# Optimization experiments

Measured on AMD Instinct MI355X. Metric: run time of the kernel, lower is better.

Reference implementation:

```python
import jax, jax.numpy as jnp
import numpy as np

ACTION_NS = [3, 3, 2, 4, 24]        # forward_back, left_right, jump, sneak_sprint, attack_...
RANGE_STARTS = [6, 8, 10, 11, 14]   # action_ranges starts (indices 0..5 are commit + camera ops)
N_ACTIONS = 37
LOGIT_DIM = 36
MIN_DELTA = 0.5 / 2**3
MAX_STEP = 20
MAX_CAMSTEP = 6
B, NUM_INPUT, HIDDEN = 32768, 1024, 2048
D_IN = NUM_INPUT + 4 + LOGIT_DIM


def setup_inputs():
    key = jax.random.key(0)
    ks = jax.random.split(key, 12)
    inp = {
        "fc_input": jax.random.normal(ks[0], (B, NUM_INPUT), jnp.float32),
        "camera": jax.random.normal(ks[1], (B, 2), jnp.float32),
        "rand_u": jax.random.uniform(ks[2], (B,), jnp.float32),
        "W1": (jax.random.normal(ks[3], (D_IN, HIDDEN), jnp.float32) / np.sqrt(D_IN)).astype(jnp.float32),
        "b1": jnp.zeros((HIDDEN,), jnp.float32),
        "W2": (jax.random.normal(ks[4], (HIDDEN, N_ACTIONS), jnp.float32) / np.sqrt(HIDDEN)).astype(jnp.float32),
        "b2": jnp.zeros((N_ACTIONS,), jnp.float32),
    }
    names = ["act_fb", "act_lr", "act_jp", "act_ss", "act_atk"]
    for i, (nm, n) in enumerate(zip(names, ACTION_NS)):
        inp[nm] = jax.random.randint(ks[5 + i], (B,), 0, n, jnp.int32)
    return inp


def _discretize_scan(camera, acts):
    # Faithful jax version of the 20-step no_grad target/input construction loop.
    nB = camera.shape[0]
    cam0, cam1 = camera[:, 0], camera[:, 1]

    def step(carry, _):
        ac, delta, rdac, dch, cam_steps, committed, norm = carry
        oh = [jax.nn.one_hot(r, n, dtype=jnp.float32) for r, n in zip(rdac, ACTION_NS)]
        inp_vec = jnp.concatenate([ac] + oh + [delta[:, None], dch.astype(jnp.float32)[:, None]], axis=1)  # [B,40]
        norm = norm + (~committed).astype(jnp.float32)
        commit = ((jnp.abs(cam0) < 1e-5) & (jnp.abs(cam1) < 1e-5)) | (cam_steps >= MAX_CAMSTEP)
        for r, a in zip(rdac, acts):
            commit = commit & (r == a)
        dac = jnp.zeros((nB,), jnp.int32)
        modified = commit
        new_rdac = []
        for r, a, rs in zip(rdac, acts, RANGE_STARTS):
            disc = (~modified) & (r != a)
            dac = jnp.where(disc & (a == 0), r - 1 + rs, jnp.where(disc, a - 1 + rs, dac))
            new_rdac.append(jnp.where(disc, a, r))
            modified = modified | disc
        d2 = delta * 2.0
        # NOTE: original torch code compares cam[:,1] against ac[:,0]; bug preserved.
        dmask = (~modified) & (~dch) & ((jnp.abs(cam0 - ac[:, 0]) > d2) | (jnp.abs(cam1 - ac[:, 0]) > d2))
        dac = jnp.where(dmask, 5, dac)
        delta = jnp.where(dmask, jnp.clip(d2, -0.5, 0.5), delta)
        modified = modified | dmask
        sx = jnp.where(cam0 < ac[:, 0], -1.0, 1.0)
        sy = jnp.where(cam1 < ac[:, 1], -1.0, 1.0)
        quad = jnp.where(sx < 0, jnp.where(sy < 0, 1, 3), jnp.where(sy < 0, 2, 4)).astype(jnp.int32)
        dac = jnp.where(~modified, quad, dac)
        move = jnp.stack([sx, sy], axis=1) * delta[:, None]
        ac = jnp.where((~modified)[:, None], ac + move, ac)
        delta = jnp.where(~modified, delta * 0.5, delta)
        dch = dch | (~modified)
        cam_steps = cam_steps + (~modified).astype(jnp.int32)
        committed = committed | commit
        return (ac, delta, tuple(new_rdac), dch, cam_steps, committed, norm), (inp_vec, dac)

    init = (jnp.zeros((nB, 2), jnp.float32),
            jnp.full((nB,), MIN_DELTA, jnp.float32),
            tuple(jnp.zeros((nB,), jnp.int32) for _ in ACTION_NS),
            jnp.zeros((nB,), bool),
            jnp.zeros((nB,), jnp.int32),
            jnp.zeros((nB,), bool),
            jnp.zeros((nB,), jnp.float32))
    carry, (all_inputs, all_dacs) = jax.lax.scan(step, init, None, length=MAX_STEP)
    return all_inputs, all_dacs, carry[-1]  # [T,B,40], [T,B], norm [B]


def reference(fc_input, camera, rand_u, W1, b1, W2, b2, act_fb, act_lr, act_jp, act_ss, act_atk):
    acts = (act_fb, act_lr, act_jp, act_ss, act_atk)
    all_inputs, all_dacs, norm = _discretize_scan(camera, acts)
    rand_sam = jnp.minimum((rand_u * norm).astype(jnp.int32), MAX_STEP - 1)  # sample an uncommitted step
    idx = jnp.arange(fc_input.shape[0])
    sel = jax.lax.stop_gradient(all_inputs[rand_sam, idx])  # [B,40]
    tgt = jax.lax.stop_gradient(all_dacs[rand_sam, idx])    # [B]
    x = jnp.concatenate([fc_input, sel], axis=1)
    h = x @ W1 + b1
    h = h * jax.nn.sigmoid(h)  # swish
    logits = h @ W2 + b2
    logp = jax.nn.log_softmax(logits, axis=-1)
    loss = -jnp.take_along_axis(logp, tgt[:, None], axis=1)[:, 0]  # per-sample CE (reduction='none')
    return loss
```

## Files before the change

### kernel.cpp

```cpp
#include <hip/hip_runtime.h>
#include <hip/hip_bf16.h>
#include <stdint.h>

#define B_ROWS 32768
#define NUM_IN 1024
#define D_PAD2 1088
#define HID    2048
#define NPAD   64

typedef __attribute__((ext_vector_type(8))) short bf16x8;
typedef __attribute__((ext_vector_type(4))) float f32x4;
typedef unsigned short ushort_t;

__device__ __forceinline__ unsigned short f2bf(float f){
  union { float f; uint32_t u; } x; x.f = f;
  uint32_t u = x.u;
  return (unsigned short)((u + 0x7FFFu + ((u >> 16) & 1u)) >> 16);
}

__device__ __forceinline__ void gload16(const void* g, void* l){
  __builtin_amdgcn_global_load_lds((const __attribute__((address_space(1))) void*)g,
                                   (__attribute__((address_space(3))) void*)l, 16, 0, 0);
}

__device__ __forceinline__ int disc_step(
    float cam0, float cam1, const int a[5],
    float& ac0, float& ac1, float& delta,
    int r[5], bool& dch, int& cam_steps, bool& committed, float& norm)
{
  const int RS[5] = {6, 8, 10, 11, 14};
  norm += committed ? 0.0f : 1.0f;
  bool commit = ((fabsf(cam0) < 1e-5f) && (fabsf(cam1) < 1e-5f)) || (cam_steps >= 6);
  #pragma unroll
  for (int i = 0; i < 5; ++i) commit = commit && (r[i] == a[i]);
  int dac = 0;
  bool modified = commit;
  #pragma unroll
  for (int i = 0; i < 5; ++i){
    bool disc = (!modified) && (r[i] != a[i]);
    if (disc){
      dac = (a[i] == 0) ? (r[i] - 1 + RS[i]) : (a[i] - 1 + RS[i]);
      r[i] = a[i];
      modified = true;
    }
  }
  float d2 = delta * 2.0f;
  bool dmask = (!modified) && (!dch) &&
               ((fabsf(cam0 - ac0) > d2) || (fabsf(cam1 - ac0) > d2));
  if (dmask){ dac = 5; delta = fminf(d2, 0.5f); modified = true; }
  if (!modified){
    float sx = (cam0 < ac0) ? -1.0f : 1.0f;
    float sy = (cam1 < ac1) ? -1.0f : 1.0f;
    dac = (sx < 0.0f) ? ((sy < 0.0f) ? 1 : 3) : ((sy < 0.0f) ? 2 : 4);
    ac0 += sx * delta; ac1 += sy * delta;
    delta *= 0.5f;
    dch = true;
    cam_steps += 1;
  }
  committed = committed || commit;
  return dac;
}

__global__ void k_prep(const float* __restrict__ fc, const float* __restrict__ W1,
                       const float* __restrict__ W2,
                       const float* __restrict__ camera, const float* __restrict__ rand_u,
                       const int* __restrict__ afb, const int* __restrict__ alr,
                       const int* __restrict__ ajp, const int* __restrict__ ass,
                       const int* __restrict__ aat,
                       unsigned short* __restrict__ xb, unsigned short* __restrict__ w1t,
                       unsigned short* __restrict__ w2t, int* __restrict__ tgt)
{
  __shared__ float lt[64][65];
  const int b = blockIdx.x;
  const int tid = threadIdx.x;
  if (b < 16384){
    int gid = b * 256 + tid;
    int row = gid >> 7;
    int c   = gid & 127;
    const float4* p = (const float4*)(fc + (size_t)row * NUM_IN + c * 8);
    float4 f0 = p[0], f1 = p[1];
    uint4 pk;
    pk.x = (uint32_t)f2bf(f0.x) | ((uint32_t)f2bf(f0.y) << 16);
    pk.y = (uint32_t)f2bf(f0.z) | ((uint32_t)f2bf(f0.w) << 16);
    pk.z = (uint32_t)f2bf(f1.x) | ((uint32_t)f2bf(f1.y) << 16);
    pk.w = (uint32_t)f2bf(f1.z) | ((uint32_t)f2bf(f1.w) << 16);
    *(uint4*)(xb + (size_t)row * D_PAD2 + c * 8) = pk;
    return;
  }
  if (b < 16928){
    const int bi = b - 16384;
    const int kt = bi % 17, nt = bi / 17;
    const int k0 = kt * 64, n0 = nt * 64;
    const int c = tid & 63, rq = tid >> 6;
    #pragma unroll
    for (int rr = 0; rr < 16; ++rr){
      const int r = rr * 4 + rq;
      const int k = k0 + r;
      lt[r][c] = (k < 1064) ? W1[(size_t)k * HID + n0 + c] : 0.0f;
    }
    __syncthreads();
    #pragma unroll
    for (int rr = 0; rr < 16; ++rr){
      const int r = rr * 4 + rq;
      w1t[(size_t)(n0 + r) * D_PAD2 + k0 + c] = f2bf(lt[c][r]);
    }
    return;
  }
  if (b < 17440){
    int idx = (b - 16928) * 256 + tid;
    int n = idx >> 11;
    int k = idx & (HID - 1);
    float v = (n < 37) ? W2[(size_t)k * 37 + n] : 0.0f;
    w2t[idx] = f2bf(v);
    return;
  }
  int row = (b - 17440) * 256 + tid;
  float cam0 = camera[2*row], cam1 = camera[2*row + 1];
  int a[5] = { afb[row], alr[row], ajp[row], ass[row], aat[row] };

  float ac0 = 0.f, ac1 = 0.f, delta = 0.0625f, norm = 0.f;
  int r[5] = {0,0,0,0,0};
  bool dch = false, committed = false; int cam_steps = 0;
  for (int t = 0; t < 20; ++t)
    disc_step(cam0, cam1, a, ac0, ac1, delta, r, dch, cam_steps, committed, norm);

  int rs = (int)(rand_u[row] * norm);
  if (rs > 19) rs = 19;
  if (rs < 0) rs = 0;

  ac0 = 0.f; ac1 = 0.f; delta = 0.0625f; norm = 0.f;
  r[0]=r[1]=r[2]=r[3]=r[4]=0; dch = false; committed = false; cam_steps = 0;
  for (int t = 0; t < rs; ++t)
    disc_step(cam0, cam1, a, ac0, ac1, delta, r, dch, cam_steps, committed, norm);

  float vec[40];
  #pragma unroll
  for (int j = 0; j < 40; ++j) vec[j] = 0.0f;
  vec[0] = ac0; vec[1] = ac1;
  const int offs[5] = {2, 5, 8, 10, 14};
  #pragma unroll
  for (int i = 0; i < 5; ++i) vec[offs[i] + r[i]] = 1.0f;
  vec[38] = delta; vec[39] = dch ? 1.0f : 0.0f;

  int dac = disc_step(cam0, cam1, a, ac0, ac1, delta, r, dch, cam_steps, committed, norm);
  tgt[row] = dac;

  unsigned short* o = xb + (size_t)row * D_PAD2 + NUM_IN;
  #pragma unroll
  for (int j = 0; j < 40; ++j) o[j] = f2bf(vec[j]);
  #pragma unroll
  for (int j = 40; j < 64; ++j) o[j] = 0;
}

#define LDS_A0 0
#define LDS_A1 16384
#define LDS_B0 32768
#define LDS_B1 49152

#define STAGE(G, REG, ROW0, KT, HALF) do { \
    const ushort_t* s0_ = (G) + (size_t)((ROW0) + (HALF)*128 + srow) * D_PAD2 + ((KT) << 6) + scol; \
    gload16(s0_, lds + (REG) + (HALF)*8192 + t*8); \
    gload16(s0_ + (size_t)64 * D_PAD2, lds + (REG) + (HALF)*8192 + 4096 + t*8); \
  } while(0)

#define LDA_(REG, MH) do { \
    _Pragma("unroll") for (int mi_ = 0; mi_ < 4; ++mi_){ \
      const int row_ = arow_base + (MH)*64 + mi_*16; \
      _Pragma("unroll") for (int kk_ = 0; kk_ < 2; ++kk_) \
        aR[mi_][kk_] = *(const bf16x8*)(lds + (REG) + row_*64 + (((kk_*4+lg)^axor)<<3)); \
    } \
  } while(0)

#define LDB_(REG, NH, BR) do { \
    _Pragma("unroll") for (int ni_ = 0; ni_ < 2; ++ni_){ \
      const int row_ = brow_base + (NH)*32 + ni_*16; \
      _Pragma("unroll") for (int kk_ = 0; kk_ < 2; ++kk_) \
        BR[ni_][kk_] = *(const bf16x8*)(lds + (REG) + row_*64 + (((kk_*4+lg)^axor)<<3)); \
    } \
  } while(0)

#define MMA(MH, NH, BR) do { \
    __builtin_amdgcn_s_setprio(1); \
    _Pragma("unroll") for (int mi_ = 0; mi_ < 4; ++mi_) \
    _Pragma("unroll") for (int ni_ = 0; ni_ < 2; ++ni_) \
    _Pragma("unroll") for (int kk_ = 0; kk_ < 2; ++kk_) \
      acc[(MH)*4+mi_][(NH)*2+ni_] = __builtin_amdgcn_mfma_f32_16x16x32_bf16( \
          aR[mi_][kk_], BR[ni_][kk_], acc[(MH)*4+mi_][(NH)*2+ni_], 0, 0, 0); \
    __builtin_amdgcn_s_setprio(0); \
  } while(0)

#define BAR() __builtin_amdgcn_s_barrier()
#define LGKM0()      asm volatile("s_waitcnt lgkmcnt(0)" ::: "memory")
#define WAIT_VM6()   asm volatile("s_waitcnt vmcnt(6)" ::: "memory")
#define WAIT_VM0()   asm volatile("s_waitcnt vmcnt(0)" ::: "memory")

__global__ __launch_bounds__(512, 2) void k_gemm1(const ushort_t* __restrict__ xb,
                                                  const ushort_t* __restrict__ w1t,
                                                  const ushort_t* __restrict__ w2t,
                                                  const float* __restrict__ b1,
                                                  float* __restrict__ pbuf)
{
  __shared__ ushort_t lds[65536];
  const int t = threadIdx.x;
  const int lane = t & 63;
  const int wid = t >> 6, wm = wid >> 2, wn = wid & 3;
  const int lr = lane & 15, lg = lane >> 4;

  const int bid = blockIdx.x;
  const int swz = (bid & 7) * 128 + (bid >> 3);
  const int brow = (swz >> 3) << 8;
  const int bcol = (swz & 7) << 8;

  const int srow = t >> 3;
  const int scol = ((t & 7) ^ (srow & 7)) << 3;

  const int axor = lr & 7;
  const int arow_base = wm*128 + lr;
  const int brow_base = wn*64 + lr;

  f32x4 acc[8][4] = {};
  bf16x8 aR[4][2], bR0[2][2], bR1[2][2];

  STAGE(xb,  LDS_A0, brow, 0, 0);  STAGE(xb,  LDS_A0, brow, 0, 1);
  STAGE(w1t, LDS_B0, bcol, 0, 0);  STAGE(w1t, LDS_B0, bcol, 0, 1);
  STAGE(xb,  LDS_A1, brow, 1, 0);
  STAGE(w1t, LDS_B1, bcol, 1, 0);  STAGE(w1t, LDS_B1, bcol, 1, 1);
  WAIT_VM6();
  BAR();

  for (int i = 0; i < 8; ++i){
    const int c1 = 2*i + 1;
    const int n0 = 2*i + 2;
    const int n1 = (2*i + 3 <= 16) ? 2*i + 3 : 16;

    LDA_(LDS_A0, 0); LDB_(LDS_B0, 0, bR0); LDB_(LDS_B0, 1, bR1);
    STAGE(xb, LDS_A1, brow, c1, 1);
    BAR(); LGKM0();
    MMA(0, 0, bR0);
    BAR();
    STAGE(w1t, LDS_B0, bcol, n0, 0);
    BAR();
    MMA(0, 1, bR1);
    BAR();
    LDA_(LDS_A0, 1);
    STAGE(w1t, LDS_B0, bcol, n0, 1);
    BAR(); LGKM0();
    MMA(1, 0, bR0);
    BAR();
    STAGE(xb, LDS_A0, brow, n0, 0);
    WAIT_VM6();
    BAR();
    MMA(1, 1, bR1);
    BAR();
    LDA_(LDS_A1, 0); LDB_(LDS_B1, 0, bR0); LDB_(LDS_B1, 1, bR1);
    STAGE(xb, LDS_A0, brow, n0, 1);
    BAR(); LGKM0();
    MMA(0, 0, bR0);
    BAR();
    STAGE(w1t, LDS_B1, bcol, n1, 0);
    BAR();
    MMA(0, 1, bR1);
    BAR();
    LDA_(LDS_A1, 1);
    STAGE(w1t, LDS_B1, bcol, n1, 1);
    BAR(); LGKM0();
    MMA(1, 0, bR0);
    BAR();
    STAGE(xb, LDS_A1, brow, n1, 0);
    WAIT_VM6();
    BAR();
    MMA(1, 1, bR1);
    BAR();
  }

  LDA_(LDS_A0, 0); LDB_(LDS_B0, 0, bR0); LDB_(LDS_B0, 1, bR1);
  LGKM0();
  MMA(0, 0, bR0); MMA(0, 1, bR1);
  LDA_(LDS_A0, 1);
  LGKM0();
  MMA(1, 0, bR0); MMA(1, 1, bR1);

  bf16x8 w2fA[4][4];
  #pragma unroll
  for (int ks = 0; ks < 4; ++ks)
    #pragma unroll
    for (int ni = 0; ni < 4; ++ni)
      w2fA[ks][ni] = *(const bf16x8*)(w2t + (size_t)(ni*16 + lr) * HID + bcol + ks*32 + lg*8);

  WAIT_VM0();
  BAR();

  float b1v[4];
  #pragma unroll
  for (int ni = 0; ni < 4; ++ni) b1v[ni] = b1[bcol + wn*64 + ni*16 + lr];

  #pragma unroll
  for (int mi = 0; mi < 8; ++mi){
    #pragma unroll
    for (int ni = 0; ni < 4; ++ni){
      const int col = wn*64 + ni*16 + lr;
      #pragma unroll
      for (int i2 = 0; i2 < 4; ++i2){
        const int row = wm*128 + mi*16 + lg*4 + i2;
        float v = acc[mi][ni][i2] + b1v[ni];
        float s = v / (1.0f + __expf(-v));
        const int chunk = (col >> 3) ^ (row & 7);
        lds[row*256 + chunk*8 + (col & 7)] = f2bf(s);
      }
    }
  }
  __syncthreads();

  bf16x8 w2fB[4][4];
  #pragma unroll
  for (int ks = 0; ks < 4; ++ks)
    #pragma unroll
    for (int ni = 0; ni < 4; ++ni)
      w2fB[ks][ni] = *(const bf16x8*)(w2t + (size_t)(ni*16 + lr) * HID + bcol + (ks+4)*32 + lg*8);

  const int rb = wid * 32;
  f32x4 acc2[2][4] = {};
  #pragma unroll
  for (int ks = 0; ks < 8; ++ks){
    bf16x8 a2[2];
    #pragma unroll
    for (int m = 0; m < 2; ++m){
      const int row = rb + m*16 + lr;
      a2[m] = *(const bf16x8*)(lds + row*256 + (((ks*4+lg) ^ (lr & 7)) << 3));
    }
    #pragma unroll
    for (int m = 0; m < 2; ++m)
      #pragma unroll
      for (int ni = 0; ni < 4; ++ni)
        acc2[m][ni] = __builtin_amdgcn_mfma_f32_16x16x32_bf16(
            a2[m], (ks < 4) ? w2fA[ks & 3][ni] : w2fB[ks & 3][ni], acc2[m][ni], 0, 0, 0);
  }

  const int cb = bcol >> 8;
  #pragma unroll
  for (int m = 0; m < 2; ++m)
    #pragma unroll
    for (int ni = 0; ni < 4; ++ni)
      #pragma unroll
      for (int i2 = 0; i2 < 4; ++i2){
        const int r = brow + rb + m*16 + lg*4 + i2;
        pbuf[((size_t)cb << 21) + ((size_t)r << 6) + ni*16 + lr] = acc2[m][ni][i2];
      }
}

__global__ __launch_bounds__(256) void k_red(const float* __restrict__ pbuf,
                                             const float* __restrict__ b2,
                                             const int* __restrict__ tgt,
                                             float* __restrict__ loss)
{
  const int lane = threadIdx.x & 63, w = threadIdx.x >> 6;
  const int row0 = blockIdx.x * 128 + w * 32;
  const float bias = (lane < 37) ? b2[lane] : 0.0f;
  for (int i = 0; i < 32; ++i){
    const int r = row0 + i;
    float s = 0.0f;
    #pragma unroll
    for (int cb = 0; cb < 8; ++cb)
      s += pbuf[((size_t)cb << 21) + ((size_t)r << 6) + lane];
    float x = (lane < 37) ? (s + bias) : -1e30f;
    float m = x;
    #pragma unroll
    for (int off = 1; off < 64; off <<= 1) m = fmaxf(m, __shfl_xor(m, off, 64));
    float e = __expf(x - m);
    float se = e;
    #pragma unroll
    for (int off = 1; off < 64; off <<= 1) se += __shfl_xor(se, off, 64);
    const int tg = tgt[r];
    const float pick = __shfl(x, tg, 64);
    if (lane == 0) loss[r] = m + __logf(se) - pick;
  }
}

extern "C" void kernel_launch(void* const* d_in, const int* in_sizes, int n_in,
                              void* d_out, int out_size, void* d_ws, size_t ws_size,
                              hipStream_t stream)
{
  (void)in_sizes; (void)n_in; (void)out_size; (void)ws_size;
  const float* fc  = (const float*)d_in[0];
  const float* cam = (const float*)d_in[1];
  const float* ru  = (const float*)d_in[2];
  const float* W1  = (const float*)d_in[3];
  const float* b1  = (const float*)d_in[4];
  const float* W2  = (const float*)d_in[5];
  const float* b2  = (const float*)d_in[6];
  const int* afb = (const int*)d_in[7];
  const int* alr = (const int*)d_in[8];
  const int* ajp = (const int*)d_in[9];
  const int* ass = (const int*)d_in[10];
  const int* aat = (const int*)d_in[11];
  float* loss = (float*)d_out;

  char* ws = (char*)d_ws;
  unsigned short* xb  = (unsigned short*)(ws);
  unsigned short* w1t = (unsigned short*)(ws + 71303168);
  unsigned short* w2t = (unsigned short*)(ws + 75759616);
  int*            tgt = (int*)           (ws + 76021760);
  float*          pbuf= (float*)         (ws + 76152832);

  k_prep<<<17568, 256, 0, stream>>>(fc, W1, W2, cam, ru, afb, alr, ajp, ass, aat,
                                    xb, w1t, w2t, tgt);
  k_gemm1<<<(B_ROWS/256) * (HID/256), 512, 0, stream>>>(xb, w1t, w2t, b1, pbuf);
  k_red  <<<B_ROWS / 128, 256, 0, stream>>>(pbuf, b2, tgt, loss);
}
```

Baseline: 269.6 us.

## Reschedule GEMM1 LDS loads and global staging; precompute swizzled LDS base pointers

The k-loop schedule of the first GEMM is reworked. Per-lane swizzled LDS base addresses are computed once as byte pointers, so each fragment load becomes a base plus a constant offset. Loads of the second B fragment half are deferred to the phase that consumes them, and A-tile staging moves into the loop so each sub-phase issues one global-to-LDS copy. Wait counts change to vmcnt(4), with an lgkmcnt(8) partial wait added. The goal is to spread memory traffic more evenly between MFMA bursts and cut address arithmetic, at the risk of exposing load latency or creating subtle LDS reuse hazards.

```diff
diff --git a/kernel.cpp b/kernel.cpp
--- a/kernel.cpp
+++ b/kernel.cpp
@@ -163,20 +163,16 @@
     gload16(s0_ + (size_t)64 * D_PAD2, lds + (REG) + (HALF)*8192 + 4096 + t*8); \
   } while(0)
 
-#define LDA_(REG, MH) do { \
-    _Pragma("unroll") for (int mi_ = 0; mi_ < 4; ++mi_){ \
-      const int row_ = arow_base + (MH)*64 + mi_*16; \
-      _Pragma("unroll") for (int kk_ = 0; kk_ < 2; ++kk_) \
-        aR[mi_][kk_] = *(const bf16x8*)(lds + (REG) + row_*64 + (((kk_*4+lg)^axor)<<3)); \
-    } \
+#define LDA_(BUF, MH) do { \
+    _Pragma("unroll") for (int mi_ = 0; mi_ < 4; ++mi_) \
+    _Pragma("unroll") for (int kk_ = 0; kk_ < 2; ++kk_) \
+      aR[mi_][kk_] = *(const bf16x8*)(aBk[kk_] + (BUF)*32768 + ((MH)*64 + mi_*16)*128); \
   } while(0)
 
-#define LDB_(REG, NH, BR) do { \
-    _Pragma("unroll") for (int ni_ = 0; ni_ < 2; ++ni_){ \
-      const int row_ = brow_base + (NH)*32 + ni_*16; \
-      _Pragma("unroll") for (int kk_ = 0; kk_ < 2; ++kk_) \
-        BR[ni_][kk_] = *(const bf16x8*)(lds + (REG) + row_*64 + (((kk_*4+lg)^axor)<<3)); \
-    } \
+#define LDB_(BUF, NH, BR) do { \
+    _Pragma("unroll") for (int ni_ = 0; ni_ < 2; ++ni_) \
+    _Pragma("unroll") for (int kk_ = 0; kk_ < 2; ++kk_) \
+      BR[ni_][kk_] = *(const bf16x8*)(bBk[kk_] + (BUF)*32768 + ((NH)*32 + ni_*16)*128); \
   } while(0)
 
 #define MMA(MH, NH, BR) do { \
@@ -190,9 +186,10 @@
   } while(0)
 
 #define BAR() __builtin_amdgcn_s_barrier()
-#define LGKM0()      asm volatile("s_waitcnt lgkmcnt(0)" ::: "memory")
-#define WAIT_VM6()   asm volatile("s_waitcnt vmcnt(6)" ::: "memory")
-#define WAIT_VM0()   asm volatile("s_waitcnt vmcnt(0)" ::: "memory")
+#define LGKM0()    asm volatile("s_waitcnt lgkmcnt(0)" ::: "memory")
+#define LGKM8()    asm volatile("s_waitcnt lgkmcnt(8)" ::: "memory")
+#define WAIT_VM4() asm volatile("s_waitcnt vmcnt(4)" ::: "memory")
+#define WAIT_VM0() asm volatile("s_waitcnt vmcnt(0)" ::: "memory")
 
 __global__ __launch_bounds__(512, 2) void k_gemm1(const ushort_t* __restrict__ xb,
                                                   const ushort_t* __restrict__ w1t,
@@ -218,14 +215,20 @@
   const int arow_base = wm*128 + lr;
   const int brow_base = wn*64 + lr;
 
+  const char* aBk[2];
+  const char* bBk[2];
+  aBk[0] = (const char*)lds + arow_base*128 + (((0*4+lg)^axor) << 4);
+  aBk[1] = (const char*)lds + arow_base*128 + (((1*4+lg)^axor) << 4);
+  bBk[0] = (const char*)lds + 65536 + brow_base*128 + (((0*4+lg)^axor) << 4);
+  bBk[1] = (const char*)lds + 65536 + brow_base*128 + (((1*4+lg)^axor) << 4);
+
   f32x4 acc[8][4] = {};
   bf16x8 aR[4][2], bR0[2][2], bR1[2][2];
 
   STAGE(xb,  LDS_A0, brow, 0, 0);  STAGE(xb,  LDS_A0, brow, 0, 1);
   STAGE(w1t, LDS_B0, bcol, 0, 0);  STAGE(w1t, LDS_B0, bcol, 0, 1);
-  STAGE(xb,  LDS_A1, brow, 1, 0);
   STAGE(w1t, LDS_B1, bcol, 1, 0);  STAGE(w1t, LDS_B1, bcol, 1, 1);
-  WAIT_VM6();
+  WAIT_VM4();
   BAR();
 
   for (int i = 0; i < 8; ++i){
@@ -233,50 +236,54 @@
     const int n0 = 2*i + 2;
     const int n1 = (2*i + 3 <= 16) ? 2*i + 3 : 16;
 
-    LDA_(LDS_A0, 0); LDB_(LDS_B0, 0, bR0); LDB_(LDS_B0, 1, bR1);
+    LDA_(0, 0); LDB_(0, 0, bR0);
+    STAGE(xb, LDS_A1, brow, c1, 0);
+    LGKM8();
+    BAR(); LGKM0();
+    MMA(0, 0, bR0);
+    BAR();
+    LDB_(0, 1, bR1);
     STAGE(xb, LDS_A1, brow, c1, 1);
     BAR(); LGKM0();
+    MMA(0, 1, bR1);
+    BAR();
+    LDA_(0, 1);
+    STAGE(w1t, LDS_B0, bcol, n0, 0);
+    BAR(); LGKM0();
+    MMA(1, 0, bR0);
+    BAR();
+    STAGE(w1t, LDS_B0, bcol, n0, 1);
+    WAIT_VM4();
+    BAR();
+    MMA(1, 1, bR1);
+    BAR();
+    LDA_(1, 0); LDB_(1, 0, bR0);
+    STAGE(xb, LDS_A0, brow, n0, 0);
+    LGKM8();
+    BAR(); LGKM0();
     MMA(0, 0, bR0);
     BAR();
-    STAGE(w1t, LDS_B0, bcol, n0, 0);
-    BAR();
+    LDB_(1, 1, bR1);
+    STAGE(xb, LDS_A0, brow, n0, 1);
+    BAR(); LGKM0();
     MMA(0, 1, bR1);
     BAR();
-    LDA_(LDS_A0, 1);
-    STAGE(w1t, LDS_B0, bcol, n0, 1);
+    LDA_(1, 1);
+    STAGE(w1t, LDS_B1, bcol, n1, 0);
     BAR(); LGKM0();
     MMA(1, 0, bR0);
     BAR();
-    STAGE(xb, LDS_A0, brow, n0, 0);
-    WAIT_VM6();
+    STAGE(w1t, LDS_B1, bcol, n1, 1);
+    WAIT_VM4();
     BAR();
     MMA(1, 1, bR1);
     BAR();
-    LDA_(LDS_A1, 0); LDB_(LDS_B1, 0, bR0); LDB_(LDS_B1, 1, bR1);
-    STAGE(xb, LDS_A0, brow, n0, 1);
-    BAR(); LGKM0();
-    MMA(0, 0, bR0);
-    BAR();
-    STAGE(w1t, LDS_B1, bcol, n1, 0);
-    BAR();
-    MMA(0, 1, bR1);
-    BAR();
-    LDA_(LDS_A1, 1);
-    STAGE(w1t, LDS_B1, bcol, n1, 1);
-    BAR(); LGKM0();
-    MMA(1, 0, bR0);
-    BAR();
-    STAGE(xb, LDS_A1, brow, n1, 0);
-    WAIT_VM6();
-    BAR();
-    MMA(1, 1, bR1);
-    BAR();
-  }
-
-  LDA_(LDS_A0, 0); LDB_(LDS_B0, 0, bR0); LDB_(LDS_B0, 1, bR1);
+  }
+
+  LDA_(0, 0); LDB_(0, 0, bR0); LDB_(0, 1, bR1);
   LGKM0();
   MMA(0, 0, bR0); MMA(0, 1, bR1);
-  LDA_(LDS_A0, 1);
+  LDA_(0, 1);
   LGKM0();
   MMA(1, 0, bR0); MMA(1, 1, bR1);
 
```

Result: no change. 269.0 us (-0.2%).
